# Optimization experiments

Measured on AMD Instinct MI355X. Metric: run time of the kernel, lower is better.

The kernel has to match this reference:

```python
import jax, jax.numpy as jnp
import numpy as np

N = 50000
E = 640000
H = 128


def setup_inputs() -> dict:
    key = jax.random.key(0)
    ks = jax.random.split(key, 16)
    s = 0.02
    return {
        "x": jax.random.uniform(ks[0], (N, 1), dtype=jnp.float32),
        "pre_h": jax.random.normal(ks[1], (N, H), dtype=jnp.float32),
        "edge_index": jax.random.randint(ks[2], (2, E), 0, N, dtype=jnp.int32),
        "edge_attr": jax.random.uniform(ks[3], (E, 1), dtype=jnp.float32),
        # encoder: Linear(1+H, H)
        "W_enc": jax.random.normal(ks[4], (1 + H, H), dtype=jnp.float32) * s,
        "b_enc": jnp.zeros((H,), dtype=jnp.float32),
        # message: Linear(2H+1, H)
        "W_M": jax.random.normal(ks[5], (2 * H + 1, H), dtype=jnp.float32) * s,
        "b_M": jnp.zeros((H,), dtype=jnp.float32),
        # update: Linear(2H, H)
        "W_U": jax.random.normal(ks[6], (2 * H, H), dtype=jnp.float32) * s,
        "b_U": jnp.zeros((H,), dtype=jnp.float32),
        # decoder: Linear(2H, 1)
        "W_dec": jax.random.normal(ks[7], (2 * H, 1), dtype=jnp.float32) * s,
        "b_dec": jnp.zeros((1,), dtype=jnp.float32),
        # terminator: Linear(2H, 1)
        "W_term": jax.random.normal(ks[8], (2 * H, 1), dtype=jnp.float32) * s,
        "b_term": jnp.zeros((1,), dtype=jnp.float32),
    }


def reference(x, pre_h, edge_index, edge_attr,
              W_enc, b_enc, W_M, b_M, W_U, b_U,
              W_dec, b_dec, W_term, b_term):
    n = x.shape[0]
    # Encoder: z = relu(Linear([x, pre_h]))  -> [N, H]
    z = jax.nn.relu(jnp.concatenate([x, pre_h], axis=-1) @ W_enc + b_enc)

    # MPNN processor (PyG flow source_to_target: row=src j, col=dst i)
    src, dst = edge_index[0], edge_index[1]
    z_i = z[dst]  # [E, H]
    z_j = z[src]  # [E, H]
    m = jax.nn.relu(jnp.concatenate([z_i, z_j, edge_attr], axis=-1) @ W_M + b_M)
    agg = jax.ops.segment_max(m, dst, num_segments=n)
    # PyG fills nodes with no incoming edges with 0 for max aggregation;
    # messages are >= 0 (relu) so clamping at 0 matches exactly.
    agg = jnp.maximum(agg, jnp.float32(0.0))
    h = jax.nn.relu(jnp.concatenate([z, agg], axis=-1) @ W_U + b_U)

    # Decoder: y = Linear([z, h]) -> [N, 1]
    y = jnp.concatenate([z, h], axis=-1) @ W_dec + b_dec

    # Terminator
    h_mean = jnp.mean(h, axis=0, keepdims=True)              # [1, H]
    hm = jnp.broadcast_to(h_mean, h.shape)                   # [N, H]
    t = jnp.concatenate([h, hm], axis=-1) @ W_term + b_term  # [N, 1]
    tau = jnp.mean(t, axis=0, keepdims=True)                 # [1, 1]

    return h, y, tau
```

## Files before the change

### kernel.cpp

```cpp
#include <hip/hip_runtime.h>

#define DEVINL __device__ __forceinline__
#define BCAP 64
#define NREP 64

typedef __attribute__((ext_vector_type(8))) short short8;
typedef __attribute__((ext_vector_type(4))) float f32x4;
typedef __attribute__((ext_vector_type(4))) unsigned short ushort4v;
typedef __attribute__((ext_vector_type(8))) unsigned short ushort8v;

DEVINL unsigned short f2bf(float f) {
    unsigned u = __float_as_uint(f);
    u += 0x7fffu + ((u >> 16) & 1u);
    return (unsigned short)(u >> 16);
}
DEVINL float bf2f(unsigned short s) { return __uint_as_float(((unsigned)s) << 16); }

__global__ __launch_bounds__(256) void k_prep(
    const float* __restrict__ Wenc, const float* __restrict__ WM,
    const float* __restrict__ WU,
    unsigned short* __restrict__ WencT, unsigned short* __restrict__ WM1T,
    unsigned short* __restrict__ WM2T, unsigned short* __restrict__ WUT,
    const int* __restrict__ ei, const float* __restrict__ attr,
    int* __restrict__ cnt, int2* __restrict__ bucket, int E)
{
    if (blockIdx.x < 64) {
        int tid = blockIdx.x * 256 + threadIdx.x;
        const int nt = 64 * 256;
        for (int i = tid; i < 128 * 128; i += nt) {
            int c = i >> 7, k = i & 127;
            WencT[c * 128 + k] = f2bf(Wenc[(1 + k) * 128 + c]);
            WM1T[c * 128 + k]  = f2bf(WM[k * 128 + c]);
            WM2T[c * 128 + k]  = f2bf(WM[(128 + k) * 128 + c]);
        }
        for (int i = tid; i < 128 * 256; i += nt) {
            int c = i >> 8, k = i & 255;
            WUT[c * 256 + k] = f2bf(WU[k * 128 + c]);
        }
    } else {
        int e = (blockIdx.x - 64) * 256 + threadIdx.x;
        if (e >= E) return;
        int src = ei[e];
        int dst = ei[E + e];
        float a = attr[e];
        int slot = atomicAdd(&cnt[dst], 1);
        if (slot < BCAP)
            bucket[(size_t)dst * BCAP + slot] = make_int2(src, __float_as_int(a));
    }
}


__global__ __launch_bounds__(256) void k_zpq(
    const float* __restrict__ x, const float* __restrict__ preh,
    const unsigned short* __restrict__ WencT, const float* __restrict__ Wenc,
    const float* __restrict__ benc,
    const unsigned short* __restrict__ WM1T, const unsigned short* __restrict__ WM2T,
    unsigned short* __restrict__ zb, unsigned short* __restrict__ Pb,
    unsigned short* __restrict__ Qb, int N)
{
    __shared__ __align__(16) unsigned short zl[16][136];
    int t = threadIdx.x;
    int wave = t >> 6, lane = t & 63;
    int m = lane & 15, quad = lane >> 4;
    int node = blockIdx.x * 16 + m;
    bool valid = node < N;
    int nodec = min(node, N - 1);
    f32x4 acc[2] = {(f32x4)0.f, (f32x4)0.f};
    const float* arow = preh + (size_t)nodec * 128;
#pragma unroll
    for (int kc = 0; kc < 4; ++kc) {
        int k0 = kc * 32 + quad * 8;
        float4 f0 = *(const float4*)(arow + k0);
        float4 f1 = *(const float4*)(arow + k0 + 4);
        short8 bfrag;
        bfrag[0] = (short)f2bf(f0.x); bfrag[1] = (short)f2bf(f0.y);
        bfrag[2] = (short)f2bf(f0.z); bfrag[3] = (short)f2bf(f0.w);
        bfrag[4] = (short)f2bf(f1.x); bfrag[5] = (short)f2bf(f1.y);
        bfrag[6] = (short)f2bf(f1.z); bfrag[7] = (short)f2bf(f1.w);
#pragma unroll
        for (int tt = 0; tt < 2; ++tt) {
            int t8 = wave * 2 + tt;
            short8 afrag = *(const short8*)(WencT + (size_t)(t8 * 16 + m) * 128 + k0);
            acc[tt] = __builtin_amdgcn_mfma_f32_16x16x32_bf16(afrag, bfrag, acc[tt], 0, 0, 0);
        }
    }
    float xv = x[nodec];
#pragma unroll
    for (int tt = 0; tt < 2; ++tt) {
        int col = (wave * 2 + tt) * 16 + quad * 4;
        float4 w0v = *(const float4*)(Wenc + col);
        float4 bv  = *(const float4*)(benc + col);
        ushort4v o;
        o[0] = f2bf(fmaxf(acc[tt][0] + xv * w0v.x + bv.x, 0.f));
        o[1] = f2bf(fmaxf(acc[tt][1] + xv * w0v.y + bv.y, 0.f));
        o[2] = f2bf(fmaxf(acc[tt][2] + xv * w0v.z + bv.z, 0.f));
        o[3] = f2bf(fmaxf(acc[tt][3] + xv * w0v.w + bv.w, 0.f));
        if (valid) *(ushort4v*)(zb + (size_t)node * 128 + col) = o;
        *(ushort4v*)&zl[m][col] = o;
    }
    __syncthreads();
    f32x4 aP[2] = {(f32x4)0.f, (f32x4)0.f};
    f32x4 aQ[2] = {(f32x4)0.f, (f32x4)0.f};
#pragma unroll
    for (int kc = 0; kc < 4; ++kc) {
        int k0 = kc * 32 + quad * 8;
        short8 bfrag = *(const short8*)&zl[m][k0];
#pragma unroll
        for (int tt = 0; tt < 2; ++tt) {
            int t8 = wave * 2 + tt;
            size_t wo = (size_t)(t8 * 16 + m) * 128 + k0;
            short8 a1 = *(const short8*)(WM1T + wo);
            aP[tt] = __builtin_amdgcn_mfma_f32_16x16x32_bf16(a1, bfrag, aP[tt], 0, 0, 0);
            short8 a2 = *(const short8*)(WM2T + wo);
            aQ[tt] = __builtin_amdgcn_mfma_f32_16x16x32_bf16(a2, bfrag, aQ[tt], 0, 0, 0);
        }
    }
    if (!valid) return;
    unsigned short* prow = Pb + (size_t)node * 128;
    unsigned short* qrow = Qb + (size_t)node * 128;
#pragma unroll
    for (int tt = 0; tt < 2; ++tt) {
        int col = (wave * 2 + tt) * 16 + quad * 4;
        ushort4v op, oq;
        op[0] = f2bf(aP[tt][0]); op[1] = f2bf(aP[tt][1]);
        op[2] = f2bf(aP[tt][2]); op[3] = f2bf(aP[tt][3]);
        oq[0] = f2bf(aQ[tt][0]); oq[1] = f2bf(aQ[tt][1]);
        oq[2] = f2bf(aQ[tt][2]); oq[3] = f2bf(aQ[tt][3]);
        *(ushort4v*)(prow + col) = op;
        *(ushort4v*)(qrow + col) = oq;
    }
}

__global__ __launch_bounds__(256) void k_aggh(
    const unsigned short* __restrict__ zb, const unsigned short* __restrict__ Pb,
    const unsigned short* __restrict__ Qb, const int2* __restrict__ bucket,
    const int* __restrict__ cnt, const float* __restrict__ w3,
    const float* __restrict__ bM, const unsigned short* __restrict__ WUT,
    const float* __restrict__ bU, const float* __restrict__ Wd,
    const float* __restrict__ bd, float* __restrict__ h,
    float* __restrict__ y, float* __restrict__ hsumR, int N)
{
    __shared__ __align__(16) unsigned short al[16][136];
    __shared__ float ys[4][16];
    __shared__ float hsb[128];
    int t = threadIdx.x;
    {
        int il = t >> 4, lane16 = t & 15, c0 = lane16 * 8;
        int i = blockIdx.x * 16 + il;
        int ic = min(i, N - 1);
        int deg = min(cnt[ic], BCAP);
        const int2* b = bucket + (size_t)ic * BCAP;
        float w[8], acc[8];
        {
            float4 wa = *(const float4*)(w3 + c0), wb = *(const float4*)(w3 + c0 + 4);
            w[0] = wa.x; w[1] = wa.y; w[2] = wa.z; w[3] = wa.w;
            w[4] = wb.x; w[5] = wb.y; w[6] = wb.z; w[7] = wb.w;
        }
        const float NI = __uint_as_float(0xff800000u);
#pragma unroll
        for (int u = 0; u < 8; ++u) acc[u] = NI;
        int j = 0;
        for (; j + 3 < deg; j += 4) {
            int2 e0 = b[j], e1 = b[j + 1], e2 = b[j + 2], e3 = b[j + 3];
            short8 q0 = *(const short8*)(Qb + (size_t)e0.x * 128 + c0);
            short8 q1 = *(const short8*)(Qb + (size_t)e1.x * 128 + c0);
            short8 q2 = *(const short8*)(Qb + (size_t)e2.x * 128 + c0);
            short8 q3 = *(const short8*)(Qb + (size_t)e3.x * 128 + c0);
            float a0 = __int_as_float(e0.y), a1 = __int_as_float(e1.y);
            float a2 = __int_as_float(e2.y), a3 = __int_as_float(e3.y);
#pragma unroll
            for (int u = 0; u < 8; ++u) {
                acc[u] = fmaxf(acc[u], fmaf(a0, w[u], bf2f((unsigned short)q0[u])));
                acc[u] = fmaxf(acc[u], fmaf(a1, w[u], bf2f((unsigned short)q1[u])));
                acc[u] = fmaxf(acc[u], fmaf(a2, w[u], bf2f((unsigned short)q2[u])));
                acc[u] = fmaxf(acc[u], fmaf(a3, w[u], bf2f((unsigned short)q3[u])));
            }
        }
        for (; j < deg; ++j) {
            int2 e0 = b[j];
            float a0 = __int_as_float(e0.y);
            short8 q0 = *(const short8*)(Qb + (size_t)e0.x * 128 + c0);
#pragma unroll
            for (int u = 0; u < 8; ++u)
                acc[u] = fmaxf(acc[u], fmaf(a0, w[u], bf2f((unsigned short)q0[u])));
        }
        short8 p = *(const short8*)(Pb + (size_t)ic * 128 + c0);
        float4 ba = *(const float4*)(bM + c0), bb = *(const float4*)(bM + c0 + 4);
        float bm[8] = {ba.x, ba.y, ba.z, ba.w, bb.x, bb.y, bb.z, bb.w};
        ushort8v o;
#pragma unroll
        for (int u = 0; u < 8; ++u)
            o[u] = f2bf(fmaxf(bf2f((unsigned short)p[u]) + bm[u] + acc[u], 0.f));
        *(ushort8v*)&al[il][c0] = o;
    }
    __syncthreads();
    int wave = t >> 6, lane = t & 63;
    int m = lane & 15, quad = lane >> 4;
    int node = blockIdx.x * 16 + m;
    bool valid = node < N;
    int nodec = min(node, N - 1);
    f32x4 acc[2] = {(f32x4)0.f, (f32x4)0.f};
    float py = 0.f;
    const unsigned short* arow = zb + (size_t)nodec * 128;
#pragma unroll
    for (int kc = 0; kc < 8; ++kc) {
        int k0 = kc * 32 + quad * 8;
        short8 bfrag;
        if (kc < 4) {
            bfrag = *(const short8*)(arow + k0);
            if (wave == 0) {
                float4 wa = *(const float4*)(Wd + k0);
                float4 wb = *(const float4*)(Wd + k0 + 4);
                py += bf2f((unsigned short)bfrag[0]) * wa.x
                    + bf2f((unsigned short)bfrag[1]) * wa.y
                    + bf2f((unsigned short)bfrag[2]) * wa.z
                    + bf2f((unsigned short)bfrag[3]) * wa.w
                    + bf2f((unsigned short)bfrag[4]) * wb.x
                    + bf2f((unsigned short)bfrag[5]) * wb.y
                    + bf2f((unsigned short)bfrag[6]) * wb.z
                    + bf2f((unsigned short)bfrag[7]) * wb.w;
            }
        } else {
            bfrag = *(const short8*)&al[m][(kc - 4) * 32 + quad * 8];
        }
#pragma unroll
        for (int tt = 0; tt < 2; ++tt) {
            int t8 = wave * 2 + tt;
            short8 afrag = *(const short8*)(WUT + (size_t)(t8 * 16 + m) * 256 + k0);
            acc[tt] = __builtin_amdgcn_mfma_f32_16x16x32_bf16(afrag, bfrag, acc[tt], 0, 0, 0);
        }
    }
    const float* Wdh = Wd + 128;
    float* orow = h + (size_t)nodec * 128;
#pragma unroll
    for (int tt = 0; tt < 2; ++tt) {
        int col = (wave * 2 + tt) * 16 + quad * 4;
        float4 bv = *(const float4*)(bU + col);
        float4 o;
        o.x = valid ? fmaxf(acc[tt][0] + bv.x, 0.f) : 0.f;
        o.y = valid ? fmaxf(acc[tt][1] + bv.y, 0.f) : 0.f;
        o.z = valid ? fmaxf(acc[tt][2] + bv.z, 0.f) : 0.f;
        o.w = valid ? fmaxf(acc[tt][3] + bv.w, 0.f) : 0.f;
        if (valid) *(float4*)(orow + col) = o;
        float4 wd = *(const float4*)(Wdh + col);
        py += o.x * wd.x + o.y * wd.y + o.z * wd.z + o.w * wd.w;
        float4 s = o;
#pragma unroll
        for (int mask = 1; mask <= 8; mask <<= 1) {
            s.x += __shfl_xor(s.x, mask, 64);
            s.y += __shfl_xor(s.y, mask, 64);
            s.z += __shfl_xor(s.z, mask, 64);
            s.w += __shfl_xor(s.w, mask, 64);
        }
        if (m == 0) *(float4*)&hsb[col] = s;
    }
    py += __shfl_xor(py, 16, 64);
    py += __shfl_xor(py, 32, 64);
    if (lane < 16) ys[wave][lane] = py;
    __syncthreads();
    if (t < 16 && blockIdx.x * 16 + t < N)
        y[blockIdx.x * 16 + t] = ys[0][t] + ys[1][t] + ys[2][t] + ys[3][t] + bd[0];
    if (t < 128)
        atomicAdd(&hsumR[(blockIdx.x & (NREP - 1)) * 128 + t], hsb[t]);
}

__global__ __launch_bounds__(128) void k_tau(
    const float* __restrict__ hsumR, const float* __restrict__ Wt,
    const float* __restrict__ bt, float* __restrict__ tau, int N)
{
    __shared__ float sd[128];
    int t = threadIdx.x;
    float s = 0.f;
#pragma unroll
    for (int r = 0; r < NREP; ++r) s += hsumR[r * 128 + t];
    float v = s * (1.f / (float)N) * (Wt[t] + Wt[128 + t]);
    sd[t] = v;
    __syncthreads();
    for (int o = 64; o > 0; o >>= 1) {
        if (t < o) sd[t] += sd[t + o];
        __syncthreads();
    }
    if (t == 0) tau[0] = sd[0] + bt[0];
}

extern "C" void kernel_launch(void* const* d_in, const int* in_sizes, int n_in,
                              void* d_out, int out_size, void* d_ws, size_t ws_size,
                              hipStream_t stream)
{
    const float* x     = (const float*)d_in[0];
    const float* preh  = (const float*)d_in[1];
    const int*   ei    = (const int*)d_in[2];
    const float* attr  = (const float*)d_in[3];
    const float* Wenc  = (const float*)d_in[4];
    const float* benc  = (const float*)d_in[5];
    const float* WM    = (const float*)d_in[6];
    const float* bM    = (const float*)d_in[7];
    const float* WU    = (const float*)d_in[8];
    const float* bU    = (const float*)d_in[9];
    const float* Wd    = (const float*)d_in[10];
    const float* bd    = (const float*)d_in[11];
    const float* Wterm = (const float*)d_in[12];
    const float* bterm = (const float*)d_in[13];
    int N = in_sizes[0];
    int E = in_sizes[3];

    char* wp = (char*)d_ws;
    unsigned short* zb    = (unsigned short*)wp; wp += (size_t)N * 128 * 2;
    unsigned short* Pb    = (unsigned short*)wp; wp += (size_t)N * 128 * 2;
    unsigned short* Qb    = (unsigned short*)wp; wp += (size_t)N * 128 * 2;
    int2*           bucket= (int2*)wp;           wp += (size_t)N * BCAP * 8;
    int*            cnt   = (int*)wp;            wp += (size_t)N * 4;
    float*          hsumR = (float*)wp;          wp += NREP * 128 * 4;
    unsigned short* WencT = (unsigned short*)wp; wp += 128 * 128 * 2;
    unsigned short* WM1T  = (unsigned short*)wp; wp += 128 * 128 * 2;
    unsigned short* WM2T  = (unsigned short*)wp; wp += 128 * 128 * 2;
    unsigned short* WUT   = (unsigned short*)wp; wp += 128 * 256 * 2;

    float* hout = (float*)d_out;
    float* yout = hout + (size_t)N * 128;
    float* tau  = yout + N;

    int nb16 = (N + 15) / 16;
    hipMemsetAsync(cnt, 0, ((size_t)N + NREP * 128) * sizeof(int), stream);

    int sb = (E + 255) / 256;
    k_prep<<<64 + sb, 256, 0, stream>>>(Wenc, WM, WU, WencT, WM1T, WM2T, WUT,
                                        ei, attr, cnt, bucket, E);
    k_zpq<<<nb16, 256, 0, stream>>>(x, preh, WencT, Wenc, benc, WM1T, WM2T,
                                    zb, Pb, Qb, N);
    k_aggh<<<nb16, 256, 0, stream>>>(zb, Pb, Qb, bucket, cnt, WM + 256 * 128,
                                     bM, WUT, bU, Wd, bd, hout, yout, hsumR, N);
    k_tau<<<1, 128, 0, stream>>>(hsumR, Wterm, bterm, tau, N);
}
```

Measured before the change: 252.2 us.

## Restructure kernel pipeline: fuse edge bucketing with encoder, compute P in aggregation, fold tau

The memset is replaced by a zeroing pass inside the weight-conversion kernel. Edge bucketing now runs as extra blocks of the encoder/Q kernel instead of the prep kernel. The P projection (z @ W_M1) is no longer stored to global memory; it is recomputed with MFMA inside the aggregation kernel from z fragments held in registers, which removes the P buffer's write and read traffic. Edge lists are staged through shared memory and the gather loop is unrolled by 8 for more memory-level parallelism. The separate tau kernel is removed: the last block, found through an atomic done-counter, computes tau, at the cost of more shared memory per block and a threadfence.

```diff
diff --git a/kernel.cpp b/kernel.cpp
--- a/kernel.cpp
+++ b/kernel.cpp
@@ -7,7 +7,6 @@
 typedef __attribute__((ext_vector_type(8))) short short8;
 typedef __attribute__((ext_vector_type(4))) float f32x4;
 typedef __attribute__((ext_vector_type(4))) unsigned short ushort4v;
-typedef __attribute__((ext_vector_type(8))) unsigned short ushort8v;
 
 DEVINL unsigned short f2bf(float f) {
     unsigned u = __float_as_uint(f);
@@ -16,13 +15,12 @@
 }
 DEVINL float bf2f(unsigned short s) { return __uint_as_float(((unsigned)s) << 16); }
 
-__global__ __launch_bounds__(256) void k_prep(
+__global__ __launch_bounds__(256) void k_w(
     const float* __restrict__ Wenc, const float* __restrict__ WM,
     const float* __restrict__ WU,
     unsigned short* __restrict__ WencT, unsigned short* __restrict__ WM1T,
     unsigned short* __restrict__ WM2T, unsigned short* __restrict__ WUT,
-    const int* __restrict__ ei, const float* __restrict__ attr,
-    int* __restrict__ cnt, int2* __restrict__ bucket, int E)
+    int* __restrict__ zbase, int zn)
 {
     if (blockIdx.x < 64) {
         int tid = blockIdx.x * 256 + threadIdx.x;
@@ -38,7 +36,23 @@
             WUT[c * 256 + k] = f2bf(WU[k * 128 + c]);
         }
     } else {
-        int e = (blockIdx.x - 64) * 256 + threadIdx.x;
+        for (int i = (blockIdx.x - 64) * 256 + threadIdx.x; i < zn; i += 32 * 256)
+            zbase[i] = 0;
+    }
+}
+
+
+__global__ __launch_bounds__(256) void k_zq(
+    const float* __restrict__ x, const float* __restrict__ preh,
+    const unsigned short* __restrict__ WencT, const float* __restrict__ Wenc,
+    const float* __restrict__ benc, const unsigned short* __restrict__ WM2T,
+    unsigned short* __restrict__ zb, unsigned short* __restrict__ Qb,
+    int N, int nzq,
+    const int* __restrict__ ei, const float* __restrict__ attr,
+    int* __restrict__ cnt, int2* __restrict__ bucket, int E)
+{
+    if ((int)blockIdx.x >= nzq) {
+        int e = ((int)blockIdx.x - nzq) * 256 + threadIdx.x;
         if (e >= E) return;
         int src = ei[e];
         int dst = ei[E + e];
@@ -46,23 +60,13 @@
         int slot = atomicAdd(&cnt[dst], 1);
         if (slot < BCAP)
             bucket[(size_t)dst * BCAP + slot] = make_int2(src, __float_as_int(a));
-    }
-}
-
-
-__global__ __launch_bounds__(256) void k_zpq(
-    const float* __restrict__ x, const float* __restrict__ preh,
-    const unsigned short* __restrict__ WencT, const float* __restrict__ Wenc,
-    const float* __restrict__ benc,
-    const unsigned short* __restrict__ WM1T, const unsigned short* __restrict__ WM2T,
-    unsigned short* __restrict__ zb, unsigned short* __restrict__ Pb,
-    unsigned short* __restrict__ Qb, int N)
-{
+        return;
+    }
     __shared__ __align__(16) unsigned short zl[16][136];
     int t = threadIdx.x;
     int wave = t >> 6, lane = t & 63;
     int m = lane & 15, quad = lane >> 4;
-    int node = blockIdx.x * 16 + m;
+    int node = (int)blockIdx.x * 16 + m;
     bool valid = node < N;
     int nodec = min(node, N - 1);
     f32x4 acc[2] = {(f32x4)0.f, (f32x4)0.f};
@@ -99,7 +103,6 @@
         *(ushort4v*)&zl[m][col] = o;
     }
     __syncthreads();
-    f32x4 aP[2] = {(f32x4)0.f, (f32x4)0.f};
     f32x4 aQ[2] = {(f32x4)0.f, (f32x4)0.f};
 #pragma unroll
     for (int kc = 0; kc < 4; ++kc) {
@@ -108,106 +111,154 @@
 #pragma unroll
         for (int tt = 0; tt < 2; ++tt) {
             int t8 = wave * 2 + tt;
-            size_t wo = (size_t)(t8 * 16 + m) * 128 + k0;
-            short8 a1 = *(const short8*)(WM1T + wo);
-            aP[tt] = __builtin_amdgcn_mfma_f32_16x16x32_bf16(a1, bfrag, aP[tt], 0, 0, 0);
-            short8 a2 = *(const short8*)(WM2T + wo);
+            short8 a2 = *(const short8*)(WM2T + (size_t)(t8 * 16 + m) * 128 + k0);
             aQ[tt] = __builtin_amdgcn_mfma_f32_16x16x32_bf16(a2, bfrag, aQ[tt], 0, 0, 0);
         }
     }
     if (!valid) return;
-    unsigned short* prow = Pb + (size_t)node * 128;
     unsigned short* qrow = Qb + (size_t)node * 128;
 #pragma unroll
     for (int tt = 0; tt < 2; ++tt) {
         int col = (wave * 2 + tt) * 16 + quad * 4;
-        ushort4v op, oq;
-        op[0] = f2bf(aP[tt][0]); op[1] = f2bf(aP[tt][1]);
-        op[2] = f2bf(aP[tt][2]); op[3] = f2bf(aP[tt][3]);
+        ushort4v oq;
         oq[0] = f2bf(aQ[tt][0]); oq[1] = f2bf(aQ[tt][1]);
         oq[2] = f2bf(aQ[tt][2]); oq[3] = f2bf(aQ[tt][3]);
-        *(ushort4v*)(prow + col) = op;
         *(ushort4v*)(qrow + col) = oq;
     }
 }
 
 __global__ __launch_bounds__(256) void k_aggh(
-    const unsigned short* __restrict__ zb, const unsigned short* __restrict__ Pb,
-    const unsigned short* __restrict__ Qb, const int2* __restrict__ bucket,
-    const int* __restrict__ cnt, const float* __restrict__ w3,
-    const float* __restrict__ bM, const unsigned short* __restrict__ WUT,
+    const unsigned short* __restrict__ zb, const unsigned short* __restrict__ Qb,
+    const int2* __restrict__ bucket, const int* __restrict__ cnt,
+    const float* __restrict__ w3, const float* __restrict__ bM,
+    const unsigned short* __restrict__ WUT, const unsigned short* __restrict__ WM1T,
     const float* __restrict__ bU, const float* __restrict__ Wd,
-    const float* __restrict__ bd, float* __restrict__ h,
-    float* __restrict__ y, float* __restrict__ hsumR, int N)
+    const float* __restrict__ bd, const float* __restrict__ Wterm,
+    const float* __restrict__ bterm,
+    float* __restrict__ h, float* __restrict__ y, float* __restrict__ hsumR,
+    unsigned* __restrict__ done, float* __restrict__ tau, int N)
 {
+    __shared__ int degs[16];
+    __shared__ __align__(16) int2 eb[16][BCAP];
+    __shared__ __align__(16) float mac[16][132];
     __shared__ __align__(16) unsigned short al[16][136];
     __shared__ float ys[4][16];
     __shared__ float hsb[128];
+    __shared__ float sd[128];
+    __shared__ unsigned lastv;
+
     int t = threadIdx.x;
+    int bid16 = (int)blockIdx.x * 16;
+    int wave = t >> 6, lane = t & 63;
+    int m = lane & 15, quad = lane >> 4;
+    int node = bid16 + m;
+    bool valid = node < N;
+    int nodec = min(node, N - 1);
+
+    const unsigned short* arow = zb + (size_t)nodec * 128;
+    short8 zfr[4];
+#pragma unroll
+    for (int kc = 0; kc < 4; ++kc)
+        zfr[kc] = *(const short8*)(arow + kc * 32 + quad * 8);
+
+    if (t < 16) degs[t] = min(cnt[min(bid16 + t, N - 1)], BCAP);
+    __syncthreads();
+    for (int idx = t; idx < 16 * BCAP; idx += 256) {
+        int nd = idx >> 6, sl = idx & (BCAP - 1);
+        if (sl < degs[nd])
+            eb[nd][sl] = bucket[(size_t)min(bid16 + nd, N - 1) * BCAP + sl];
+    }
+    __syncthreads();
     {
-        int il = t >> 4, lane16 = t & 15, c0 = lane16 * 8;
-        int i = blockIdx.x * 16 + il;
-        int ic = min(i, N - 1);
-        int deg = min(cnt[ic], BCAP);
-        const int2* b = bucket + (size_t)ic * BCAP;
-        float w[8], acc[8];
+        int il = t >> 4, c0 = (t & 15) * 8;
+        int deg = degs[il];
+        float w[8];
         {
             float4 wa = *(const float4*)(w3 + c0), wb = *(const float4*)(w3 + c0 + 4);
-            w[0] = wa.x; w[1] = wa.y; w[2] = wa.z; w[3] = wa.w;
-            w[4] = wb.x; w[5] = wb.y; w[6] = wb.z; w[7] = wb.w;
+            w[0]=wa.x; w[1]=wa.y; w[2]=wa.z; w[3]=wa.w;
+            w[4]=wb.x; w[5]=wb.y; w[6]=wb.z; w[7]=wb.w;
         }
         const float NI = __uint_as_float(0xff800000u);
-#pragma unroll
-        for (int u = 0; u < 8; ++u) acc[u] = NI;
+        float a8[8];
+#pragma unroll
+        for (int u = 0; u < 8; ++u) a8[u] = NI;
         int j = 0;
+        for (; j + 7 < deg; j += 8) {
+            int2 e[8]; short8 q[8];
+#pragma unroll
+            for (int b = 0; b < 8; ++b) e[b] = eb[il][j + b];
+#pragma unroll
+            for (int b = 0; b < 8; ++b)
+                q[b] = *(const short8*)(Qb + (size_t)e[b].x * 128 + c0);
+#pragma unroll
+            for (int b = 0; b < 8; ++b) {
+                float a = __int_as_float(e[b].y);
+#pragma unroll
+                for (int u = 0; u < 8; ++u)
+                    a8[u] = fmaxf(a8[u], fmaf(a, w[u], bf2f((unsigned short)q[b][u])));
+            }
+        }
         for (; j + 3 < deg; j += 4) {
-            int2 e0 = b[j], e1 = b[j + 1], e2 = b[j + 2], e3 = b[j + 3];
+            int2 e[4]; short8 q[4];
+#pragma unroll
+            for (int b = 0; b < 4; ++b) e[b] = eb[il][j + b];
+#pragma unroll
+            for (int b = 0; b < 4; ++b)
+                q[b] = *(const short8*)(Qb + (size_t)e[b].x * 128 + c0);
+#pragma unroll
+            for (int b = 0; b < 4; ++b) {
+                float a = __int_as_float(e[b].y);
+#pragma unroll
+                for (int u = 0; u < 8; ++u)
+                    a8[u] = fmaxf(a8[u], fmaf(a, w[u], bf2f((unsigned short)q[b][u])));
+            }
+        }
+        for (; j < deg; ++j) {
+            int2 e0 = eb[il][j];
+            float a = __int_as_float(e0.y);
             short8 q0 = *(const short8*)(Qb + (size_t)e0.x * 128 + c0);
-            short8 q1 = *(const short8*)(Qb + (size_t)e1.x * 128 + c0);
-            short8 q2 = *(const short8*)(Qb + (size_t)e2.x * 128 + c0);
-            short8 q3 = *(const short8*)(Qb + (size_t)e3.x * 128 + c0);
-            float a0 = __int_as_float(e0.y), a1 = __int_as_float(e1.y);
-            float a2 = __int_as_float(e2.y), a3 = __int_as_float(e3.y);
-#pragma unroll
-            for (int u = 0; u < 8; ++u) {
-                acc[u] = fmaxf(acc[u], fmaf(a0, w[u], bf2f((unsigned short)q0[u])));
-                acc[u] = fmaxf(acc[u], fmaf(a1, w[u], bf2f((unsigned short)q1[u])));
-                acc[u] = fmaxf(acc[u], fmaf(a2, w[u], bf2f((unsigned short)q2[u])));
-                acc[u] = fmaxf(acc[u], fmaf(a3, w[u], bf2f((unsigned short)q3[u])));
+#pragma unroll
+            for (int u = 0; u < 8; ++u)
+                a8[u] = fmaxf(a8[u], fmaf(a, w[u], bf2f((unsigned short)q0[u])));
+        }
+        *(f32x4*)&mac[il][c0]     = *(f32x4*)&a8[0];
+        *(f32x4*)&mac[il][c0 + 4] = *(f32x4*)&a8[4];
+    }
+    __syncthreads();
+    {
+        f32x4 accP[2] = {(f32x4)0.f, (f32x4)0.f};
+#pragma unroll
+        for (int kc = 0; kc < 4; ++kc) {
+            int k0 = kc * 32 + quad * 8;
+#pragma unroll
+            for (int tt = 0; tt < 2; ++tt) {
+                int t8 = wave * 2 + tt;
+                short8 afrag = *(const short8*)(WM1T + (size_t)(t8 * 16 + m) * 128 + k0);
+                accP[tt] = __builtin_amdgcn_mfma_f32_16x16x32_bf16(afrag, zfr[kc], accP[tt], 0, 0, 0);
             }
         }
-        for (; j < deg; ++j) {
-            int2 e0 = b[j];
-            float a0 = __int_as_float(e0.y);
-            short8 q0 = *(const short8*)(Qb + (size_t)e0.x * 128 + c0);
-#pragma unroll
-            for (int u = 0; u < 8; ++u)
-                acc[u] = fmaxf(acc[u], fmaf(a0, w[u], bf2f((unsigned short)q0[u])));
-        }
-        short8 p = *(const short8*)(Pb + (size_t)ic * 128 + c0);
-        float4 ba = *(const float4*)(bM + c0), bb = *(const float4*)(bM + c0 + 4);
-        float bm[8] = {ba.x, ba.y, ba.z, ba.w, bb.x, bb.y, bb.z, bb.w};
-        ushort8v o;
-#pragma unroll
-        for (int u = 0; u < 8; ++u)
-            o[u] = f2bf(fmaxf(bf2f((unsigned short)p[u]) + bm[u] + acc[u], 0.f));
-        *(ushort8v*)&al[il][c0] = o;
-    }
-    __syncthreads();
-    int wave = t >> 6, lane = t & 63;
-    int m = lane & 15, quad = lane >> 4;
-    int node = blockIdx.x * 16 + m;
-    bool valid = node < N;
-    int nodec = min(node, N - 1);
+#pragma unroll
+        for (int tt = 0; tt < 2; ++tt) {
+            int col = (wave * 2 + tt) * 16 + quad * 4;
+            float4 bmv = *(const float4*)(bM + col);
+            float4 mv  = *(const float4*)&mac[m][col];
+            ushort4v o;
+            o[0] = f2bf(fmaxf(accP[tt][0] + bmv.x + mv.x, 0.f));
+            o[1] = f2bf(fmaxf(accP[tt][1] + bmv.y + mv.y, 0.f));
+            o[2] = f2bf(fmaxf(accP[tt][2] + bmv.z + mv.z, 0.f));
+            o[3] = f2bf(fmaxf(accP[tt][3] + bmv.w + mv.w, 0.f));
+            *(ushort4v*)&al[m][col] = o;
+        }
+    }
+    __syncthreads();
     f32x4 acc[2] = {(f32x4)0.f, (f32x4)0.f};
     float py = 0.f;
-    const unsigned short* arow = zb + (size_t)nodec * 128;
 #pragma unroll
     for (int kc = 0; kc < 8; ++kc) {
         int k0 = kc * 32 + quad * 8;
         short8 bfrag;
         if (kc < 4) {
-            bfrag = *(const short8*)(arow + k0);
+            bfrag = zfr[kc];
             if (wave == 0) {
                 float4 wa = *(const float4*)(Wd + k0);
                 float4 wb = *(const float4*)(Wd + k0 + 4);
@@ -258,29 +309,28 @@
     py += __shfl_xor(py, 32, 64);
     if (lane < 16) ys[wave][lane] = py;
     __syncthreads();
-    if (t < 16 && blockIdx.x * 16 + t < N)
-        y[blockIdx.x * 16 + t] = ys[0][t] + ys[1][t] + ys[2][t] + ys[3][t] + bd[0];
+    if (t < 16 && bid16 + t < N)
+        y[bid16 + t] = ys[0][t] + ys[1][t] + ys[2][t] + ys[3][t] + bd[0];
     if (t < 128)
-        atomicAdd(&hsumR[(blockIdx.x & (NREP - 1)) * 128 + t], hsb[t]);
-}
-
-__global__ __launch_bounds__(128) void k_tau(
-    const float* __restrict__ hsumR, const float* __restrict__ Wt,
-    const float* __restrict__ bt, float* __restrict__ tau, int N)
-{
-    __shared__ float sd[128];
-    int t = threadIdx.x;
-    float s = 0.f;
-#pragma unroll
-    for (int r = 0; r < NREP; ++r) s += hsumR[r * 128 + t];
-    float v = s * (1.f / (float)N) * (Wt[t] + Wt[128 + t]);
-    sd[t] = v;
-    __syncthreads();
-    for (int o = 64; o > 0; o >>= 1) {
-        if (t < o) sd[t] += sd[t + o];
+        atomicAdd(&hsumR[((int)blockIdx.x & (NREP - 1)) * 128 + t], hsb[t]);
+    __threadfence();
+    if (t == 0) lastv = atomicAdd(done, 1u);
+    __syncthreads();
+    if (lastv == gridDim.x - 1) {
+        if (t < 128) {
+            float s = 0.f;
+#pragma unroll
+            for (int r = 0; r < NREP; ++r)
+                s += atomicAdd(&hsumR[r * 128 + t], 0.0f);
+            sd[t] = s * (1.f / (float)N) * (Wterm[t] + Wterm[128 + t]);
+        }
         __syncthreads();
-    }
-    if (t == 0) tau[0] = sd[0] + bt[0];
+        for (int o2 = 64; o2 > 0; o2 >>= 1) {
+            if (t < o2) sd[t] += sd[t + o2];
+            __syncthreads();
+        }
+        if (t == 0) tau[0] = sd[0] + bterm[0];
+    }
 }
 
 extern "C" void kernel_launch(void* const* d_in, const int* in_sizes, int n_in,
@@ -306,11 +356,11 @@
 
     char* wp = (char*)d_ws;
     unsigned short* zb    = (unsigned short*)wp; wp += (size_t)N * 128 * 2;
-    unsigned short* Pb    = (unsigned short*)wp; wp += (size_t)N * 128 * 2;
     unsigned short* Qb    = (unsigned short*)wp; wp += (size_t)N * 128 * 2;
     int2*           bucket= (int2*)wp;           wp += (size_t)N * BCAP * 8;
     int*            cnt   = (int*)wp;            wp += (size_t)N * 4;
     float*          hsumR = (float*)wp;          wp += NREP * 128 * 4;
+    unsigned*       done  = (unsigned*)wp;       wp += 4;
     unsigned short* WencT = (unsigned short*)wp; wp += 128 * 128 * 2;
     unsigned short* WM1T  = (unsigned short*)wp; wp += 128 * 128 * 2;
     unsigned short* WM2T  = (unsigned short*)wp; wp += 128 * 128 * 2;
@@ -321,14 +371,15 @@
     float* tau  = yout + N;
 
     int nb16 = (N + 15) / 16;
-    hipMemsetAsync(cnt, 0, ((size_t)N + NREP * 128) * sizeof(int), stream);
-
     int sb = (E + 255) / 256;
-    k_prep<<<64 + sb, 256, 0, stream>>>(Wenc, WM, WU, WencT, WM1T, WM2T, WUT,
+    int zn = N + NREP * 128 + 1;
+
+    k_w<<<96, 256, 0, stream>>>(Wenc, WM, WU, WencT, WM1T, WM2T, WUT,
+                                cnt, zn);
+    k_zq<<<nb16 + sb, 256, 0, stream>>>(x, preh, WencT, Wenc, benc, WM2T,
+                                        zb, Qb, N, nb16,
                                         ei, attr, cnt, bucket, E);
-    k_zpq<<<nb16, 256, 0, stream>>>(x, preh, WencT, Wenc, benc, WM1T, WM2T,
-                                    zb, Pb, Qb, N);
-    k_aggh<<<nb16, 256, 0, stream>>>(zb, Pb, Qb, bucket, cnt, WM + 256 * 128,
-                                     bM, WUT, bU, Wd, bd, hout, yout, hsumR, N);
-    k_tau<<<1, 128, 0, stream>>>(hsumR, Wterm, bterm, tau, N);
-}
+    k_aggh<<<nb16, 256, 0, stream>>>(zb, Qb, bucket, cnt, WM + 256 * 128, bM,
+                                     WUT, WM1T, bU, Wd, bd, Wterm, bterm,
+                                     hout, yout, hsumR, done, tau, N);
+}
```

Result: slower. 576.8 us (+128.7%).
